# Kernel tuning notes

Measured on AMD Instinct MI355X. Metric: run time of the kernel, lower is better.

## Reference

```python
import jax, jax.numpy as jnp
import numpy as np

N, C, H, W = 16, 256, 64, 64
KC, VC, HEADS = 256, 256, 8

def setup_inputs() -> dict:
    key = jax.random.key(0)
    ks = jax.random.split(key, 9)
    s = 0.02
    return {
        "x": jax.random.normal(ks[0], (N, C, H, W), dtype=jnp.float32),
        "Wk": jax.random.normal(ks[1], (KC, C), dtype=jnp.float32) * s,
        "bk": jax.random.normal(ks[2], (KC,), dtype=jnp.float32) * s,
        "Wq": jax.random.normal(ks[3], (KC, C), dtype=jnp.float32) * s,
        "bq": jax.random.normal(ks[4], (KC,), dtype=jnp.float32) * s,
        "Wv": jax.random.normal(ks[5], (VC, C), dtype=jnp.float32) * s,
        "bv": jax.random.normal(ks[6], (VC,), dtype=jnp.float32) * s,
        "Wr": jax.random.normal(ks[7], (C, VC), dtype=jnp.float32) * s,
        "br": jax.random.normal(ks[8], (C,), dtype=jnp.float32) * s,
    }

def reference(x, Wk, bk, Wq, bq, Wv, bv, Wr, br):
    n, c, h, w = x.shape
    hw = h * w
    hk = KC // HEADS   # per-head key channels
    hv = VC // HEADS   # per-head value channels
    # 1x1 convs as channel matmuls
    keys = jnp.einsum('oi,nihw->nohw', Wk, x) + bk[None, :, None, None]
    queries = jnp.einsum('oi,nihw->nohw', Wq, x) + bq[None, :, None, None]
    values = jnp.einsum('oi,nihw->nohw', Wv, x) + bv[None, :, None, None]
    # split heads: (n, heads, ch_per_head, hw)
    k = keys.reshape(n, HEADS, hk, hw)
    q = queries.reshape(n, HEADS, hk, hw)
    v = values.reshape(n, HEADS, hv, hw)
    k = jax.nn.softmax(k, axis=3)   # softmax over spatial positions
    q = jax.nn.softmax(q, axis=2)   # softmax over key channels
    # context: (n, heads, hk, hv)
    ctx = jnp.einsum('nhkl,nhvl->nhkv', k, v)
    # attended: (n, heads, hv, hw)
    att = jnp.einsum('nhkv,nhkl->nhvl', ctx, q)
    agg = att.reshape(n, VC, h, w)
    out = jnp.einsum('ov,nvhw->nohw', Wr, agg) + br[None, :, None, None] + x
    return out
```

## Files before the change

### kernel.cpp

```cpp
#include <hip/hip_runtime.h>

#define NB   16
#define CD   256
#define HWD  4096

typedef __attribute__((ext_vector_type(8))) short short8;
typedef __attribute__((ext_vector_type(4))) float f32x4;

static __device__ __forceinline__ float b2f(unsigned short u) {
  union { unsigned int i; float f; } x; x.i = ((unsigned int)u) << 16; return x.f;
}
static __device__ __forceinline__ unsigned short f2b(float f) {
  union { float f; unsigned int i; } x; x.f = f;
  return (unsigned short)((x.i + 0x7fffu + ((x.i >> 16) & 1u)) >> 16);
}

static __device__ __forceinline__ void gload16(const void* g, const unsigned short* l) {
  __builtin_amdgcn_global_load_lds(
      (const __attribute__((address_space(1))) void*)g,
      (__attribute__((address_space(3))) void*)l, 16, 0, 0);
}

__global__ __launch_bounds__(256)
void prep_kernel(const float* __restrict__ Wk, const float* __restrict__ Wq,
                 const float* __restrict__ Wv, unsigned short* __restrict__ Wc)
{
  int e4 = blockIdx.x * 256 + threadIdx.x;
  int base = e4 * 4;
  int w = base >> 16, off = base & 65535;
  const float* W = (w == 0) ? Wk : (w == 1) ? Wq : Wv;
  f32x4 v = *(const f32x4*)(W + off);
  unsigned int lo = (unsigned int)f2b(v.x) | ((unsigned int)f2b(v.y) << 16);
  unsigned int hi = (unsigned int)f2b(v.z) | ((unsigned int)f2b(v.w) << 16);
  *(uint2*)(Wc + base) = make_uint2(lo, hi);
}

__global__ __launch_bounds__(256)
void xt_kernel(const float* __restrict__ x, unsigned short* __restrict__ xT)
{
  __shared__ __align__(16) unsigned short T[64 * 80];
  const int t = threadIdx.x;
  const int l0 = blockIdx.x * 64, c0 = blockIdx.y * 64, n = blockIdx.z;
  const float* xn = x + (size_t)n * CD * HWD;
#pragma unroll
  for (int i = 0; i < 4; ++i) {
    int idx = t + i * 256;
    int c = idx >> 4, l4 = (idx & 15) * 4;
    f32x4 v = *(const f32x4*)(xn + (size_t)(c0 + c) * HWD + l0 + l4);
    T[(l4 + 0) * 80 + c] = f2b(v.x);
    T[(l4 + 1) * 80 + c] = f2b(v.y);
    T[(l4 + 2) * 80 + c] = f2b(v.z);
    T[(l4 + 3) * 80 + c] = f2b(v.w);
  }
  __syncthreads();
  unsigned short* dst = xT + ((size_t)n * HWD + l0) * CD + c0;
#pragma unroll
  for (int i = 0; i < 2; ++i) {
    int e = t + i * 256;
    int lr = e >> 3, c8 = (e & 7) * 8;
    *(short8*)(dst + (size_t)lr * CD + c8) = *(const short8*)(T + lr * 80 + c8);
  }
}

__global__ __launch_bounds__(256, 4)
void kqv_kernel(const unsigned short* __restrict__ Wc,
                const unsigned short* __restrict__ xT,
                const float* __restrict__ bk, const float* __restrict__ bq,
                const float* __restrict__ bv,
                unsigned short* __restrict__ ekeys,
                unsigned short* __restrict__ qsmT,
                unsigned short* __restrict__ vals)
{
  __shared__ __align__(16) unsigned short smem[17408];

  const int t  = threadIdx.x;
  const int lt = blockIdx.x;
  const int mt = blockIdx.y;
  const int n  = blockIdx.z;
  const int l0 = lt * 128;
  const int m0 = mt * 128;
  const int wsel = m0 >> 8;
  const int ocbase = m0 & 255;

  const unsigned short* Ag  = Wc;
  const unsigned short* Btn = xT + (size_t)n * HWD * CD;

  const int w = t >> 6, lane = t & 63;
  const int wr = (w >> 1) * 64, wc = (w & 1) * 64;
  const int lhi = lane >> 4, llo = lane & 15;

  f32x4 acc[4][4] = {};

  auto stage = [&](int buf, int ks) {
    unsigned short* As = smem + buf * 8192;
    unsigned short* Bs = As + 4096;
    const int k0 = ks * 32;
#pragma unroll
    for (int i = 0; i < 2; ++i) {
      int s   = t + i * 256;
      int row = s >> 2;
      int src = (((s ^ row) & 3)) << 3;
      gload16(Ag  + (size_t)(m0 + row) * CD + k0 + src, As + s * 8);
      gload16(Btn + (size_t)(l0 + row) * CD + k0 + src, Bs + s * 8);
    }
  };

  stage(0, 0);
  stage(1, 1);
#pragma unroll
  for (int ks = 0; ks < 8; ++ks) {
    if (ks < 7) asm volatile("s_waitcnt vmcnt(4)" ::: "memory");
    else        asm volatile("s_waitcnt vmcnt(0)" ::: "memory");
    asm volatile("s_barrier" ::: "memory");

    const unsigned short* As = smem + (ks & 1) * 8192;
    const unsigned short* Bs = As + 4096;
    const int slot = (lhi ^ (llo & 3)) * 8;
    short8 a[4], b[4];
#pragma unroll
    for (int mi = 0; mi < 4; ++mi)
      a[mi] = *(const short8*)(As + (wr + mi * 16 + llo) * 32 + slot);
#pragma unroll
    for (int ni = 0; ni < 4; ++ni)
      b[ni] = *(const short8*)(Bs + (wc + ni * 16 + llo) * 32 + slot);

    asm volatile("s_waitcnt lgkmcnt(0)" ::: "memory");
    asm volatile("s_barrier" ::: "memory");

    if (ks < 6) stage(ks & 1, ks + 2);

#pragma unroll
    for (int mi = 0; mi < 4; ++mi)
#pragma unroll
      for (int ni = 0; ni < 4; ++ni)
        acc[mi][ni] = __builtin_amdgcn_mfma_f32_16x16x32_bf16(a[mi], b[ni], acc[mi][ni], 0, 0, 0);
  }

  const float* bias = (wsel == 0) ? bk : (wsel == 1) ? bq : bv;

  if (wsel == 1) {
#pragma unroll
    for (int mi = 0; mi < 4; ++mi)
#pragma unroll
      for (int r = 0; r < 4; ++r) {
        float bb = bias[ocbase + wr + mi * 16 + lhi * 4 + r];
#pragma unroll
        for (int ni = 0; ni < 4; ++ni) acc[mi][ni][r] += bb;
      }
#pragma unroll
    for (int g = 0; g < 2; ++g) {
#pragma unroll
      for (int ni = 0; ni < 4; ++ni) {
        float m = -1e30f;
#pragma unroll
        for (int mi = 2 * g; mi < 2 * g + 2; ++mi)
#pragma unroll
          for (int r = 0; r < 4; ++r) m = fmaxf(m, acc[mi][ni][r]);
        m = fmaxf(m, __shfl_xor(m, 16));
        m = fmaxf(m, __shfl_xor(m, 32));
        float s = 0.f;
#pragma unroll
        for (int mi = 2 * g; mi < 2 * g + 2; ++mi)
#pragma unroll
          for (int r = 0; r < 4; ++r) {
            float e = __expf(acc[mi][ni][r] - m);
            acc[mi][ni][r] = e;
            s += e;
          }
        s += __shfl_xor(s, 16);
        s += __shfl_xor(s, 32);
        float inv = 1.f / s;
#pragma unroll
        for (int mi = 2 * g; mi < 2 * g + 2; ++mi)
#pragma unroll
          for (int r = 0; r < 4; ++r) acc[mi][ni][r] *= inv;
      }
    }
    unsigned short* Co2 = smem;
#pragma unroll
    for (int mi = 0; mi < 4; ++mi)
#pragma unroll
      for (int ni = 0; ni < 4; ++ni) {
        int col = wc + ni * 16 + llo;
#pragma unroll
        for (int r = 0; r < 4; ++r) {
          int row = wr + mi * 16 + lhi * 4 + r;
          Co2[col * 136 + row] = f2b(acc[mi][ni][r]);
        }
      }
    __syncthreads();
    unsigned short* dst = qsmT + ((size_t)n * HWD + l0) * CD + ocbase;
#pragma unroll
    for (int i = 0; i < 8; ++i) {
      int e = t + i * 256;
      int l = e >> 4, c8 = (e & 15) * 8;
      *(short8*)(dst + (size_t)l * CD + c8) = *(const short8*)(Co2 + l * 136 + c8);
    }
  } else {
    unsigned short* Co = smem;
#pragma unroll
    for (int mi = 0; mi < 4; ++mi)
#pragma unroll
      for (int ni = 0; ni < 4; ++ni) {
        int col = wc + ni * 16 + llo;
#pragma unroll
        for (int r = 0; r < 4; ++r) {
          int row = wr + mi * 16 + lhi * 4 + r;
          float val = acc[mi][ni][r] + bias[ocbase + row];
          if (wsel == 0) val = __expf(val);
          Co[row * 136 + col] = f2b(val);
        }
      }
    __syncthreads();
    unsigned short* dst = ((wsel == 0) ? ekeys : vals)
                          + ((size_t)(n * CD + ocbase)) * HWD + l0;
#pragma unroll
    for (int i = 0; i < 8; ++i) {
      int e = t + i * 256;
      int row = e >> 4, c8 = (e & 15) * 8;
      *(short8*)(dst + (size_t)row * HWD + c8) = *(const short8*)(Co + row * 136 + c8);
    }
  }
}

__global__ __launch_bounds__(256)
void rowsum_kernel(const unsigned short* __restrict__ ekeys,
                   float* __restrict__ stats)
{
  __shared__ float red[4];
  const int r = blockIdx.x;
  const int t = threadIdx.x;
  const unsigned short* rowp = ekeys + (size_t)r * HWD;
  float s = 0.f;
#pragma unroll
  for (int i = 0; i < 2; ++i) {
    const short8 u = *(const short8*)(rowp + t * 8 + i * 2048);
#pragma unroll
    for (int j = 0; j < 8; ++j) s += b2f((unsigned short)u[j]);
  }
#pragma unroll
  for (int off = 1; off < 64; off <<= 1) s += __shfl_xor(s, off);
  if ((t & 63) == 0) red[t >> 6] = s;
  __syncthreads();
  if (t == 0) stats[r] = 1.f / (red[0] + red[1] + red[2] + red[3]);
}

__global__ __launch_bounds__(256)
void ctx_kernel(const unsigned short* __restrict__ ekeys,
                const unsigned short* __restrict__ vals,
                const float* __restrict__ stats,
                float* __restrict__ ctxp)
{
  __shared__ float Cs[4][32][33];
  const int hf = blockIdx.x;
  const int nh = blockIdx.y;
  const int n = nh >> 3, h = nh & 7;
  const int t = threadIdx.x, w = t >> 6, lane = t & 63;
  const int lhi = lane >> 4, llo = lane & 15;
  const int lbase = hf * 512 + w * 128;

  const unsigned short* kr = ekeys + (size_t)(n * CD + h * 32) * HWD;
  const unsigned short* vr = vals + (size_t)(n * CD + h * 32) * HWD;

  float inv[2];
#pragma unroll
  for (int mi = 0; mi < 2; ++mi)
    inv[mi] = stats[n * CD + h * 32 + mi * 16 + llo];

  f32x4 acc[2][2] = {};
#pragma unroll
  for (int ks = 0; ks < 4; ++ks) {
    const int loff = lbase + ks * 32 + lhi * 8;
    short8 a[2], b[2];
#pragma unroll
    for (int mi = 0; mi < 2; ++mi) {
      const short8 u = *(const short8*)(kr + (size_t)(mi * 16 + llo) * HWD + loff);
      short8 af;
#pragma unroll
      for (int j = 0; j < 8; ++j)
        af[j] = (short)f2b(b2f((unsigned short)u[j]) * inv[mi]);
      a[mi] = af;
    }
#pragma unroll
    for (int ni = 0; ni < 2; ++ni)
      b[ni] = *(const short8*)(vr + (size_t)(ni * 16 + llo) * HWD + loff);
    acc[0][0] = __builtin_amdgcn_mfma_f32_16x16x32_bf16(a[0], b[0], acc[0][0], 0, 0, 0);
    acc[0][1] = __builtin_amdgcn_mfma_f32_16x16x32_bf16(a[0], b[1], acc[0][1], 0, 0, 0);
    acc[1][0] = __builtin_amdgcn_mfma_f32_16x16x32_bf16(a[1], b[0], acc[1][0], 0, 0, 0);
    acc[1][1] = __builtin_amdgcn_mfma_f32_16x16x32_bf16(a[1], b[1], acc[1][1], 0, 0, 0);
  }

#pragma unroll
  for (int mi = 0; mi < 2; ++mi)
#pragma unroll
    for (int ni = 0; ni < 2; ++ni)
#pragma unroll
      for (int r = 0; r < 4; ++r)
        Cs[w][mi * 16 + lhi * 4 + r][ni * 16 + llo] = acc[mi][ni][r];
  __syncthreads();
#pragma unroll
  for (int i = 0; i < 4; ++i) {
    int e = t + i * 256;
    int kc = e >> 5, vc = e & 31;
    float sum = Cs[0][kc][vc] + Cs[1][kc][vc] + Cs[2][kc][vc] + Cs[3][kc][vc];
    ctxp[((size_t)hf * 128 + nh) * 1024 + e] = sum;
  }
}

__global__ __launch_bounds__(256)
void proj_kernel(const float* __restrict__ ctxp, const float* __restrict__ Wr,
                 unsigned short* __restrict__ M)
{
  __shared__ float cs[32][33];
  const int nh = blockIdx.x;
  const int n = nh >> 3, h = nh & 7;
  const int t = threadIdx.x;
#pragma unroll
  for (int i = 0; i < 4; ++i) {
    int e = t + i * 256;
    float s = 0.f;
#pragma unroll
    for (int p = 0; p < 8; ++p)
      s += ctxp[((size_t)p * 128 + nh) * 1024 + e];
    cs[e >> 5][e & 31] = s;
  }
  __syncthreads();
  float wreg[32];
  const float* wp = Wr + (size_t)t * 256 + h * 32;
#pragma unroll
  for (int i = 0; i < 8; ++i) {
    f32x4 v = *(const f32x4*)(wp + i * 4);
    wreg[i * 4] = v.x; wreg[i * 4 + 1] = v.y; wreg[i * 4 + 2] = v.z; wreg[i * 4 + 3] = v.w;
  }
  unsigned short o16[32];
#pragma unroll
  for (int kc = 0; kc < 32; ++kc) {
    float s = 0.f;
#pragma unroll
    for (int vv = 0; vv < 32; ++vv) s += wreg[vv] * cs[kc][vv];
    o16[kc] = f2b(s);
  }
  unsigned short* mp = M + (size_t)(n * CD + t) * 256 + h * 32;
#pragma unroll
  for (int i = 0; i < 8; ++i) {
    unsigned int lo = (unsigned int)o16[i * 4]     | ((unsigned int)o16[i * 4 + 1] << 16);
    unsigned int hi = (unsigned int)o16[i * 4 + 2] | ((unsigned int)o16[i * 4 + 3] << 16);
    *(uint2*)(mp + i * 4) = make_uint2(lo, hi);
  }
}

__global__ __launch_bounds__(256, 4)
void out_kernel(const unsigned short* __restrict__ M,
                const unsigned short* __restrict__ qsmT,
                const float* __restrict__ br,
                const float* __restrict__ x,
                float* __restrict__ out)
{
  __shared__ __align__(16) unsigned short smem[16384];

  const int t  = threadIdx.x;
  const int lt = blockIdx.x;
  const int mt = blockIdx.y;
  const int n  = blockIdx.z;
  const int l0 = lt * 128, m0 = mt * 128;

  const unsigned short* Ag  = M + (size_t)n * CD * 256;
  const unsigned short* Btn = qsmT + (size_t)n * HWD * CD;

  const int w = t >> 6, lane = t & 63;
  const int wr = (w >> 1) * 64, wc = (w & 1) * 64;
  const int lhi = lane >> 4, llo = lane & 15;

  f32x4 acc[4][4] = {};

  auto stage = [&](int buf, int ks) {
    unsigned short* As = smem + buf * 8192;
    unsigned short* Bs = As + 4096;
    const int k0 = ks * 32;
#pragma unroll
    for (int i = 0; i < 2; ++i) {
      int s   = t + i * 256;
      int row = s >> 2;
      int src = (((s ^ row) & 3)) << 3;
      gload16(Ag  + (size_t)(m0 + row) * CD + k0 + src, As + s * 8);
      gload16(Btn + (size_t)(l0 + row) * CD + k0 + src, Bs + s * 8);
    }
  };

  stage(0, 0);
  stage(1, 1);
#pragma unroll
  for (int ks = 0; ks < 8; ++ks) {
    if (ks < 7) asm volatile("s_waitcnt vmcnt(4)" ::: "memory");
    else        asm volatile("s_waitcnt vmcnt(0)" ::: "memory");
    asm volatile("s_barrier" ::: "memory");

    const unsigned short* As = smem + (ks & 1) * 8192;
    const unsigned short* Bs = As + 4096;
    const int slot = (lhi ^ (llo & 3)) * 8;
    short8 a[4], b[4];
#pragma unroll
    for (int mi = 0; mi < 4; ++mi)
      a[mi] = *(const short8*)(As + (wr + mi * 16 + llo) * 32 + slot);
#pragma unroll
    for (int ni = 0; ni < 4; ++ni)
      b[ni] = *(const short8*)(Bs + (wc + ni * 16 + llo) * 32 + slot);

    asm volatile("s_waitcnt lgkmcnt(0)" ::: "memory");
    asm volatile("s_barrier" ::: "memory");

    if (ks < 6) stage(ks & 1, ks + 2);

#pragma unroll
    for (int mi = 0; mi < 4; ++mi)
#pragma unroll
      for (int ni = 0; ni < 4; ++ni)
        acc[mi][ni] = __builtin_amdgcn_mfma_f32_16x16x32_bf16(a[mi], b[ni], acc[mi][ni], 0, 0, 0);
  }

  const float* xn = x + (size_t)n * CD * HWD;
  float* on = out + (size_t)n * CD * HWD;
#pragma unroll
  for (int mi = 0; mi < 4; ++mi)
#pragma unroll
    for (int r = 0; r < 4; ++r) {
      int row = m0 + wr + mi * 16 + lhi * 4 + r;
      float bb = br[row];
#pragma unroll
      for (int ni = 0; ni < 4; ++ni) {
        int col = l0 + wc + ni * 16 + llo;
        size_t off = (size_t)row * HWD + col;
        on[off] = acc[mi][ni][r] + bb + xn[off];
      }
    }
}

extern "C" void kernel_launch(void* const* d_in, const int* in_sizes, int n_in,
                              void* d_out, int out_size, void* d_ws, size_t ws_size,
                              hipStream_t stream) {
  const float* x  = (const float*)d_in[0];
  const float* Wk = (const float*)d_in[1];
  const float* bk = (const float*)d_in[2];
  const float* Wq = (const float*)d_in[3];
  const float* bq = (const float*)d_in[4];
  const float* Wv = (const float*)d_in[5];
  const float* bv = (const float*)d_in[6];
  const float* Wr = (const float*)d_in[7];
  const float* br = (const float*)d_in[8];
  float* out = (float*)d_out;

  char* ws = (char*)d_ws;
  unsigned short* ekeys = (unsigned short*)(ws);
  unsigned short* vals  = (unsigned short*)(ws + 33554432);
  unsigned short* qsmT  = (unsigned short*)(ws + 67108864);
  float* stats          = (float*)(ws + 100663296);
  unsigned short* M     = (unsigned short*)(ws + 101744640);
  unsigned short* Wc    = (unsigned short*)(ws + 103841792);
  unsigned short* xT    = (unsigned short*)d_out;
  float* ctxp           = (float*)((char*)d_out + 33554432);

  hipLaunchKernelGGL(prep_kernel, dim3(192), dim3(256), 0, stream, Wk, Wq, Wv, Wc);
  hipLaunchKernelGGL(xt_kernel, dim3(64, 4, NB), dim3(256), 0, stream, x, xT);
  hipLaunchKernelGGL(kqv_kernel, dim3(32, 6, NB), dim3(256), 0, stream,
                     Wc, xT, bk, bq, bv, ekeys, qsmT, vals);
  hipLaunchKernelGGL(rowsum_kernel, dim3(NB * CD), dim3(256), 0, stream, ekeys, stats);
  hipLaunchKernelGGL(ctx_kernel, dim3(8, 128), dim3(256), 0, stream,
                     ekeys, vals, stats, ctxp);
  hipLaunchKernelGGL(proj_kernel, dim3(128), dim3(256), 0, stream, ctxp, Wr, M);
  hipLaunchKernelGGL(out_kernel, dim3(32, 2, NB), dim3(256), 0, stream,
                     M, qsmT, br, x, out);
}
```

Before: 131.7 us.

## Fuse key softmax row sums into KQV epilogue and defer normalization

Computes per-tile row sums of the exponentiated keys inside the KQV GEMM epilogue, writing partial sums per spatial tile to a 2D stats buffer. This removes the separate rowsum kernel, which re-read the whole ekeys tensor. The 1/sum normalization moves from the ctx kernel's bf16 inputs to the proj kernel, where it scales the reduced context rows, so ctx no longer converts and rescales keys. It adds shuffle reductions and an extra barrier pair to the KQV epilogue. Sums are now taken over fp32 values rather than rounded bf16 values, which slightly changes numerics.

```diff
diff --git a/kernel.cpp b/kernel.cpp
--- a/kernel.cpp
+++ b/kernel.cpp
@@ -69,7 +69,8 @@
                 const float* __restrict__ bv,
                 unsigned short* __restrict__ ekeys,
                 unsigned short* __restrict__ qsmT,
-                unsigned short* __restrict__ vals)
+                unsigned short* __restrict__ vals,
+                float* __restrict__ stats2d)
 {
   __shared__ __align__(16) unsigned short smem[17408];
 
@@ -197,6 +198,41 @@
       *(short8*)(dst + (size_t)l * CD + c8) = *(const short8*)(Co2 + l * 136 + c8);
     }
   } else {
+#pragma unroll
+    for (int mi = 0; mi < 4; ++mi)
+#pragma unroll
+      for (int r = 0; r < 4; ++r) {
+        float bb = bias[ocbase + wr + mi * 16 + lhi * 4 + r];
+#pragma unroll
+        for (int ni = 0; ni < 4; ++ni) {
+          float v = acc[mi][ni][r] + bb;
+          acc[mi][ni][r] = (wsel == 0) ? __expf(v) : v;
+        }
+      }
+
+    if (wsel == 0) {
+      float* redp = (float*)smem;
+#pragma unroll
+      for (int mi = 0; mi < 4; ++mi)
+#pragma unroll
+        for (int r = 0; r < 4; ++r) {
+          float s = acc[mi][0][r] + acc[mi][1][r] + acc[mi][2][r] + acc[mi][3][r];
+          s += __shfl_xor(s, 1);
+          s += __shfl_xor(s, 2);
+          s += __shfl_xor(s, 4);
+          s += __shfl_xor(s, 8);
+          if (llo == 0) redp[w * 64 + mi * 16 + lhi * 4 + r] = s;
+        }
+      __syncthreads();
+      if (t < 128) {
+        int row = t;
+        float s = redp[(row >> 6) * 128 + (row & 63)]
+                + redp[(row >> 6) * 128 + 64 + (row & 63)];
+        stats2d[(size_t)lt * 4096 + n * CD + ocbase + row] = s;
+      }
+      __syncthreads();
+    }
+
     unsigned short* Co = smem;
 #pragma unroll
     for (int mi = 0; mi < 4; ++mi)
@@ -206,9 +242,7 @@
 #pragma unroll
         for (int r = 0; r < 4; ++r) {
           int row = wr + mi * 16 + lhi * 4 + r;
-          float val = acc[mi][ni][r] + bias[ocbase + row];
-          if (wsel == 0) val = __expf(val);
-          Co[row * 136 + col] = f2b(val);
+          Co[row * 136 + col] = f2b(acc[mi][ni][r]);
         }
       }
     __syncthreads();
@@ -224,31 +258,8 @@
 }
 
 __global__ __launch_bounds__(256)
-void rowsum_kernel(const unsigned short* __restrict__ ekeys,
-                   float* __restrict__ stats)
-{
-  __shared__ float red[4];
-  const int r = blockIdx.x;
-  const int t = threadIdx.x;
-  const unsigned short* rowp = ekeys + (size_t)r * HWD;
-  float s = 0.f;
-#pragma unroll
-  for (int i = 0; i < 2; ++i) {
-    const short8 u = *(const short8*)(rowp + t * 8 + i * 2048);
-#pragma unroll
-    for (int j = 0; j < 8; ++j) s += b2f((unsigned short)u[j]);
-  }
-#pragma unroll
-  for (int off = 1; off < 64; off <<= 1) s += __shfl_xor(s, off);
-  if ((t & 63) == 0) red[t >> 6] = s;
-  __syncthreads();
-  if (t == 0) stats[r] = 1.f / (red[0] + red[1] + red[2] + red[3]);
-}
-
-__global__ __launch_bounds__(256)
 void ctx_kernel(const unsigned short* __restrict__ ekeys,
                 const unsigned short* __restrict__ vals,
-                const float* __restrict__ stats,
                 float* __restrict__ ctxp)
 {
   __shared__ float Cs[4][32][33];
@@ -262,25 +273,14 @@
   const unsigned short* kr = ekeys + (size_t)(n * CD + h * 32) * HWD;
   const unsigned short* vr = vals + (size_t)(n * CD + h * 32) * HWD;
 
-  float inv[2];
-#pragma unroll
-  for (int mi = 0; mi < 2; ++mi)
-    inv[mi] = stats[n * CD + h * 32 + mi * 16 + llo];
-
   f32x4 acc[2][2] = {};
 #pragma unroll
   for (int ks = 0; ks < 4; ++ks) {
     const int loff = lbase + ks * 32 + lhi * 8;
     short8 a[2], b[2];
 #pragma unroll
-    for (int mi = 0; mi < 2; ++mi) {
-      const short8 u = *(const short8*)(kr + (size_t)(mi * 16 + llo) * HWD + loff);
-      short8 af;
-#pragma unroll
-      for (int j = 0; j < 8; ++j)
-        af[j] = (short)f2b(b2f((unsigned short)u[j]) * inv[mi]);
-      a[mi] = af;
-    }
+    for (int mi = 0; mi < 2; ++mi)
+      a[mi] = *(const short8*)(kr + (size_t)(mi * 16 + llo) * HWD + loff);
 #pragma unroll
     for (int ni = 0; ni < 2; ++ni)
       b[ni] = *(const short8*)(vr + (size_t)(ni * 16 + llo) * HWD + loff);
@@ -309,12 +309,24 @@
 
 __global__ __launch_bounds__(256)
 void proj_kernel(const float* __restrict__ ctxp, const float* __restrict__ Wr,
+                 const float* __restrict__ stats2d,
                  unsigned short* __restrict__ M)
 {
   __shared__ float cs[32][33];
+  __shared__ float invs[32];
   const int nh = blockIdx.x;
   const int n = nh >> 3, h = nh & 7;
   const int t = threadIdx.x;
+
+  if (t < 32) {
+    int grow = n * CD + h * 32 + t;
+    float s = 0.f;
+#pragma unroll
+    for (int p = 0; p < 32; ++p) s += stats2d[(size_t)p * 4096 + grow];
+    invs[t] = 1.f / s;
+  }
+  __syncthreads();
+
 #pragma unroll
   for (int i = 0; i < 4; ++i) {
     int e = t + i * 256;
@@ -322,7 +334,7 @@
 #pragma unroll
     for (int p = 0; p < 8; ++p)
       s += ctxp[((size_t)p * 128 + nh) * 1024 + e];
-    cs[e >> 5][e & 31] = s;
+    cs[e >> 5][e & 31] = s * invs[e >> 5];
   }
   __syncthreads();
   float wreg[32];
@@ -453,7 +465,7 @@
   unsigned short* ekeys = (unsigned short*)(ws);
   unsigned short* vals  = (unsigned short*)(ws + 33554432);
   unsigned short* qsmT  = (unsigned short*)(ws + 67108864);
-  float* stats          = (float*)(ws + 100663296);
+  float* stats2d        = (float*)(ws + 100663296);
   unsigned short* M     = (unsigned short*)(ws + 101744640);
   unsigned short* Wc    = (unsigned short*)(ws + 103841792);
   unsigned short* xT    = (unsigned short*)d_out;
@@ -462,11 +474,11 @@
   hipLaunchKernelGGL(prep_kernel, dim3(192), dim3(256), 0, stream, Wk, Wq, Wv, Wc);
   hipLaunchKernelGGL(xt_kernel, dim3(64, 4, NB), dim3(256), 0, stream, x, xT);
   hipLaunchKernelGGL(kqv_kernel, dim3(32, 6, NB), dim3(256), 0, stream,
-                     Wc, xT, bk, bq, bv, ekeys, qsmT, vals);
-  hipLaunchKernelGGL(rowsum_kernel, dim3(NB * CD), dim3(256), 0, stream, ekeys, stats);
+                     Wc, xT, bk, bq, bv, ekeys, qsmT, vals, stats2d);
   hipLaunchKernelGGL(ctx_kernel, dim3(8, 128), dim3(256), 0, stream,
-                     ekeys, vals, stats, ctxp);
-  hipLaunchKernelGGL(proj_kernel, dim3(128), dim3(256), 0, stream, ctxp, Wr, M);
+                     ekeys, vals, ctxp);
+  hipLaunchKernelGGL(proj_kernel, dim3(128), dim3(256), 0, stream,
+                     ctxp, Wr, stats2d, M);
   hipLaunchKernelGGL(out_kernel, dim3(32, 2, NB), dim3(256), 0, stream,
                      M, qsmT, br, x, out);
 }
```

New measurement: 224.3 us. 70.3% more time.
